# Performance work log

Hardware: AMD Instinct MI355X
Metric: run time of the kernel (lower is better)

## Reference

```python
import jax, jax.numpy as jnp
import numpy as np

D_MODEL = 1024
NUM_HEAD = 16
D_HEAD = D_MODEL // NUM_HEAD
NEG_INF = -1e9


def setup_inputs() -> dict:
    key = jax.random.key(0)
    ks = jax.random.split(key, 10)
    B, S = 16, 512
    v = jax.random.normal(ks[0], (B, S, D_MODEL), dtype=jnp.float32)
    lengths = jax.random.randint(ks[1], (B,), 1, S + 1, dtype=jnp.int32)
    scale = 0.02
    Wq = jax.random.normal(ks[2], (D_MODEL, D_MODEL), dtype=jnp.float32) * scale
    bq = jnp.zeros((D_MODEL,), dtype=jnp.float32)
    Wk = jax.random.normal(ks[3], (D_MODEL, D_MODEL), dtype=jnp.float32) * scale
    bk = jnp.zeros((D_MODEL,), dtype=jnp.float32)
    Wv = jax.random.normal(ks[4], (D_MODEL, D_MODEL), dtype=jnp.float32) * scale
    bv = jnp.zeros((D_MODEL,), dtype=jnp.float32)
    Wo = jax.random.normal(ks[5], (D_MODEL, D_MODEL), dtype=jnp.float32) * scale
    bo = jnp.zeros((D_MODEL,), dtype=jnp.float32)
    return {"v": v, "lengths": lengths, "Wq": Wq, "bq": bq, "Wk": Wk,
            "bk": bk, "Wv": Wv, "bv": bv, "Wo": Wo, "bo": bo}


def reference(v, lengths, Wq, bq, Wk, bk, Wv, bv, Wo, bo):
    B, S, D = v.shape
    H, Dh = NUM_HEAD, D_HEAD
    # key-padding mask: True where key position j is valid (j < lengths[b])
    valid = jnp.arange(S)[None, :] < lengths[:, None]          # [B, S]
    # project q, k, v and split heads -> [B, H, S, Dh]
    def split_heads(x):
        return x.reshape(B, S, H, Dh).transpose(0, 2, 1, 3)
    q = split_heads(v @ Wq + bq)
    k = split_heads(v @ Wk + bk)
    val = split_heads(v @ Wv + bv)
    scores = jnp.einsum('bhqd,bhkd->bhqk', q, k) / jnp.sqrt(jnp.float32(Dh))
    scores = jnp.where(valid[:, None, None, :], scores, NEG_INF)  # mask padded keys
    attn = jax.nn.softmax(scores, axis=-1)
    out = jnp.einsum('bhqk,bhkd->bhqd', attn, val)              # [B, H, S, Dh]
    out = out.transpose(0, 2, 1, 3).reshape(B, S, D)
    return out @ Wo + bo
```

## Files before the change

### kernel.cpp

```cpp
#include <hip/hip_runtime.h>
#include <hip/hip_bf16.h>

typedef unsigned short u16;
typedef __attribute__((ext_vector_type(8))) short short8;
typedef __attribute__((ext_vector_type(4))) float f32x4;

#define B_SZ 16
#define S_SZ 512
#define D_SZ 1024
#define H_SZ 16
#define DH_SZ 64
#define M_SZ (B_SZ * S_SZ)
#define EXPSCALE 0.18033688f

__device__ __forceinline__ void gload_lds16(const void* g, void* l) {
  __builtin_amdgcn_global_load_lds(
      (const __attribute__((address_space(1))) unsigned int*)g,
      (__attribute__((address_space(3))) unsigned int*)l,
      16, 0, 0);
}

__global__ __launch_bounds__(256) void prep(
    const float* __restrict__ v, u16* __restrict__ vB,
    const float* __restrict__ W0, const float* __restrict__ W1,
    const float* __restrict__ W2, const float* __restrict__ W3,
    u16* __restrict__ T0, u16* __restrict__ T1,
    u16* __restrict__ T2, u16* __restrict__ T3) {
  __shared__ float tile[32][33];
  const int bid = blockIdx.x;
  if (bid < 8192) {
    int i = bid * 256 + threadIdx.x;
    const float4 f = *(const float4*)&v[(size_t)i * 4];
    ushort4 o; __hip_bfloat16 h;
    h = __float2bfloat16(f.x); o.x = *(u16*)&h;
    h = __float2bfloat16(f.y); o.y = *(u16*)&h;
    h = __float2bfloat16(f.z); o.z = *(u16*)&h;
    h = __float2bfloat16(f.w); o.w = *(u16*)&h;
    *(ushort4*)&vB[(size_t)i * 4] = o;
    return;
  }
  const int tb = bid - 8192;
  const int z = tb >> 10, rem = tb & 1023;
  const int by = rem >> 5, bx = rem & 31;
  const float* W; u16* T;
  switch (z) {
    case 0: W = W0; T = T0; break;
    case 1: W = W1; T = T1; break;
    case 2: W = W2; T = T2; break;
    default: W = W3; T = T3; break;
  }
  int tx = threadIdx.x & 31, ty = threadIdx.x >> 5;
  int x = bx * 32 + tx;
#pragma unroll
  for (int i = 0; i < 32; i += 8)
    tile[ty + i][tx] = W[(size_t)(by * 32 + ty + i) * 1024 + x];
  __syncthreads();
  int x2 = by * 32 + tx;
#pragma unroll
  for (int i = 0; i < 32; i += 8) {
    __hip_bfloat16 h = __float2bfloat16(tile[tx][ty + i]);
    T[(size_t)(bx * 32 + ty + i) * 1024 + x2] = *(u16*)&h;
  }
}

struct G8 {
  const u16* A; const u16* Bt;
  u16* As; u16* Bs;
  int m0, n0;
  int wave, c, quad, r7, wm, wn;
  int srow, slc8;
};

#define AS_T (128 * 64)
#define BS_T (256 * 64)

__device__ __forceinline__ void stage_a(const G8& g, int buf, int kt, int i) {
  const int grp = g.wave * 2 + i;
  gload_lds16(&g.A[(size_t)(g.m0 + grp * 8 + g.srow) * 1024 + kt * 64 + g.slc8],
              g.As + buf * AS_T + grp * 512);
}
__device__ __forceinline__ void stage_b(const G8& g, int buf, int kt, int i) {
  const int grp = g.wave * 4 + i;
  gload_lds16(&g.Bt[(size_t)(g.n0 + grp * 8 + g.srow) * 1024 + kt * 64 + g.slc8],
              g.Bs + buf * BS_T + grp * 512);
}

template<bool ST, int VM>
__device__ __forceinline__ void tile_step(const G8& g, int cur, int stg, int kt2,
                                          f32x4 acc[4][4]) {
  const u16* ab = g.As + cur * AS_T;
  const u16* bb = g.Bs + cur * BS_T;
  short8 af[4], bf[4];

  {
    const int pc = (g.quad ^ g.r7) * 8;
#pragma unroll
    for (int i = 0; i < 4; ++i) {
      af[i] = *(const short8*)&ab[(g.wm + i * 16 + g.c) * 64 + pc];
      bf[i] = *(const short8*)&bb[(g.wn + i * 16 + g.c) * 64 + pc];
    }
    if constexpr (ST) {
      stage_a(g, stg, kt2, 0);
      stage_a(g, stg, kt2, 1);
      stage_b(g, stg, kt2, 0);
    }
    __builtin_amdgcn_s_barrier();
    __builtin_amdgcn_s_setprio(1);
#pragma unroll
    for (int mi = 0; mi < 4; ++mi)
#pragma unroll
      for (int ni = 0; ni < 4; ++ni)
        acc[mi][ni] = __builtin_amdgcn_mfma_f32_16x16x32_bf16(
            af[mi], bf[ni], acc[mi][ni], 0, 0, 0);
    __builtin_amdgcn_s_setprio(0);
    __builtin_amdgcn_s_barrier();
  }

  {
    const int pc = ((4 + g.quad) ^ g.r7) * 8;
#pragma unroll
    for (int i = 0; i < 4; ++i) {
      af[i] = *(const short8*)&ab[(g.wm + i * 16 + g.c) * 64 + pc];
      bf[i] = *(const short8*)&bb[(g.wn + i * 16 + g.c) * 64 + pc];
    }
    if constexpr (ST) {
      stage_b(g, stg, kt2, 1);
      stage_b(g, stg, kt2, 2);
      stage_b(g, stg, kt2, 3);
    }
    __builtin_amdgcn_s_barrier();
    __builtin_amdgcn_s_setprio(1);
#pragma unroll
    for (int mi = 0; mi < 4; ++mi)
#pragma unroll
      for (int ni = 0; ni < 4; ++ni)
        acc[mi][ni] = __builtin_amdgcn_mfma_f32_16x16x32_bf16(
            af[mi], bf[ni], acc[mi][ni], 0, 0, 0);
    __builtin_amdgcn_s_setprio(0);
    if constexpr (VM == 6) {
      asm volatile("s_waitcnt vmcnt(6)" ::: "memory");
      __builtin_amdgcn_s_barrier();
    } else if constexpr (VM == 0) {
      asm volatile("s_waitcnt vmcnt(0)" ::: "memory");
      __builtin_amdgcn_s_barrier();
    }
  }
}

__device__ __forceinline__ void gemm_core8(
    const u16* __restrict__ A, const u16* __restrict__ Bt,
    u16* AsB, u16* BsB, int m0, int n0, f32x4 acc[4][4]) {
  const int tid = threadIdx.x;
  const int lane = tid & 63;
  G8 g;
  g.A = A; g.Bt = Bt; g.As = AsB; g.Bs = BsB;
  g.m0 = m0; g.n0 = n0;
  g.wave = tid >> 6;
  g.c = lane & 15; g.quad = lane >> 4; g.r7 = g.c & 7;
  g.wm = (g.wave >> 2) * 64;
  g.wn = (g.wave & 3) * 64;
  g.srow = lane >> 3;
  g.slc8 = ((lane & 7) ^ g.srow) * 8;

  stage_a(g, 0, 0, 0); stage_a(g, 0, 0, 1);
  stage_b(g, 0, 0, 0); stage_b(g, 0, 0, 1); stage_b(g, 0, 0, 2); stage_b(g, 0, 0, 3);
  stage_a(g, 1, 1, 0); stage_a(g, 1, 1, 1);
  stage_b(g, 1, 1, 0); stage_b(g, 1, 1, 1); stage_b(g, 1, 1, 2); stage_b(g, 1, 1, 3);
  asm volatile("s_waitcnt vmcnt(6)" ::: "memory");
  __builtin_amdgcn_s_barrier();

  int cur = 0, stg = 2;
#pragma unroll 1
  for (int t = 0; t < 14; ++t) {
    tile_step<true, 6>(g, cur, stg, t + 2, acc);
    cur = (cur == 2) ? 0 : cur + 1;
    stg = (stg == 2) ? 0 : stg + 1;
  }
  tile_step<false, 0>(g, cur, 0, 0, acc);
  tile_step<false, -1>(g, 0, 0, 0, acc);
}

__global__ __launch_bounds__(512, 2) void gemm_qkv(
    const u16* __restrict__ A,
    const u16* __restrict__ BtQ, const u16* __restrict__ BtK, const u16* __restrict__ BtV,
    const float* __restrict__ bq, const float* __restrict__ bk, const float* __restrict__ bv,
    u16* __restrict__ Qo, u16* __restrict__ Kt, u16* __restrict__ Vt) {
  __shared__ u16 As[3][AS_T];
  __shared__ u16 Bs[3][BS_T];
  const int z = blockIdx.z;
  const u16* Bt = (z == 0) ? BtQ : (z == 1) ? BtK : BtV;
  const float* bias = (z == 0) ? bq : (z == 1) ? bk : bv;
  const int m0 = blockIdx.x * 128, n0 = blockIdx.y * 256;

  f32x4 acc[4][4];
#pragma unroll
  for (int i = 0; i < 4; ++i)
#pragma unroll
    for (int j = 0; j < 4; ++j) acc[i][j] = f32x4{0.f, 0.f, 0.f, 0.f};

  gemm_core8(A, Bt, &As[0][0], &Bs[0][0], m0, n0, acc);

  const int lane = threadIdx.x & 63, wave = threadIdx.x >> 6;
  const int wm = (wave >> 2) * 64, wn = (wave & 3) * 64;
  const int c = lane & 15, quad = lane >> 4;
#pragma unroll
  for (int ni = 0; ni < 4; ++ni) {
    int n = n0 + wn + ni * 16 + c;
    float bval = bias[n];
#pragma unroll
    for (int mi = 0; mi < 4; ++mi) {
      int mb = m0 + wm + mi * 16 + quad * 4;
      if (z == 2) {
        int bb = mb >> 9, s = mb & 511, hh = n >> 6, d = n & 63;
        ushort4 st;
        __hip_bfloat16 h0 = __float2bfloat16(acc[mi][ni][0] + bval); st.x = *(u16*)&h0;
        __hip_bfloat16 h1 = __float2bfloat16(acc[mi][ni][1] + bval); st.y = *(u16*)&h1;
        __hip_bfloat16 h2 = __float2bfloat16(acc[mi][ni][2] + bval); st.z = *(u16*)&h2;
        __hip_bfloat16 h3 = __float2bfloat16(acc[mi][ni][3] + bval); st.w = *(u16*)&h3;
        *(ushort4*)&Vt[(((size_t)(bb * 16 + hh) * 64 + d) << 9) + s] = st;
      } else {
#pragma unroll
        for (int r = 0; r < 4; ++r) {
          int m = mb + r;
          float val = acc[mi][ni][r] + bval;
          __hip_bfloat16 hb = __float2bfloat16(val);
          if (z == 0) {
            Qo[(size_t)m * 1024 + n] = *(u16*)&hb;
          } else {
            int bb = m >> 9, s = m & 511, hh = n >> 6, d = n & 63;
            Kt[(((size_t)(bb * 16 + hh) * 512 + s) << 6) + d] = *(u16*)&hb;
          }
        }
      }
    }
  }
}

__global__ __launch_bounds__(512, 2) void gemm_out(
    const u16* __restrict__ A, const u16* __restrict__ Bt,
    const float* __restrict__ bias, float* __restrict__ Cf) {
  __shared__ u16 As[3][AS_T];
  __shared__ u16 Bs[3][BS_T];
  const int m0 = blockIdx.x * 128, n0 = blockIdx.y * 256;

  f32x4 acc[4][4];
#pragma unroll
  for (int i = 0; i < 4; ++i)
#pragma unroll
    for (int j = 0; j < 4; ++j) acc[i][j] = f32x4{0.f, 0.f, 0.f, 0.f};

  gemm_core8(A, Bt, &As[0][0], &Bs[0][0], m0, n0, acc);

  const int lane = threadIdx.x & 63, wave = threadIdx.x >> 6;
  const int wm = (wave >> 2) * 64, wn = (wave & 3) * 64;
  const int c = lane & 15, quad = lane >> 4;
#pragma unroll
  for (int ni = 0; ni < 4; ++ni) {
    int n = n0 + wn + ni * 16 + c;
    float bval = bias[n];
#pragma unroll
    for (int mi = 0; mi < 4; ++mi) {
#pragma unroll
      for (int r = 0; r < 4; ++r) {
        int m = m0 + wm + mi * 16 + quad * 4 + r;
        Cf[(size_t)m * 1024 + n] = acc[mi][ni][r] + bval;
      }
    }
  }
}

__global__ __launch_bounds__(256) void attn_v6(
    const u16* __restrict__ Q, const u16* __restrict__ Kt,
    const u16* __restrict__ Vt, const int* __restrict__ lengths,
    u16* __restrict__ O) {
  const int qc = blockIdx.x, h = blockIdx.y, b = blockIdx.z;
  const int t = threadIdx.x;
  const int lane = t & 63, wave = t >> 6;
  const int c = lane & 15, quad = lane >> 4;
  const int kb = quad * 8;
  const int len = lengths[b];
  const int q0 = qc * 128 + wave * 32;

  __shared__ __align__(16) u16 Ks[64 * 64];
  __shared__ __align__(16) u16 Vs[64 * 64];
  __shared__ __align__(16) u16 Pt[4][32 * 72];

  const size_t bBase = (size_t)b * (S_SZ * D_SZ);
  const size_t hBase = ((size_t)(b * H_SZ + h)) * (S_SZ * DH_SZ);

  short8 aq[2][2];
#pragma unroll
  for (int qt = 0; qt < 2; ++qt) {
    aq[qt][0] = *(const short8*)&Q[bBase + (size_t)(q0 + qt * 16 + c) * 1024 + h * 64 + kb];
    aq[qt][1] = *(const short8*)&Q[bBase + (size_t)(q0 + qt * 16 + c) * 1024 + h * 64 + 32 + kb];
  }

  const int srow = lane >> 3;
  const int slc = (lane & 7) ^ srow;

  float rs[2] = {0.f, 0.f};
  f32x4 o[2][4];
#pragma unroll
  for (int qt = 0; qt < 2; ++qt)
#pragma unroll
    for (int i = 0; i < 4; ++i) o[qt][i] = f32x4{0.f, 0.f, 0.f, 0.f};

  const int kmax = (len + 63) & ~63;
  for (int k0 = 0; k0 < kmax; k0 += 64) {
    __syncthreads();
#pragma unroll
    for (int g = 0; g < 2; ++g) {
      const int rb = (wave * 2 + g) * 8;
      gload_lds16(&Kt[hBase + (size_t)(k0 + rb + srow) * 64 + slc * 8],
                  &Ks[(wave * 2 + g) * 512]);
      gload_lds16(&Vt[hBase + (size_t)(rb + srow) * 512 + k0 + slc * 8],
                  &Vs[(wave * 2 + g) * 512]);
    }
    __syncthreads();

#pragma unroll
    for (int sub = 0; sub < 4; ++sub) {
      const int row = sub * 16 + c;
      short8 bk0 = *(const short8*)&Ks[row * 64 + ((quad ^ (c & 7))) * 8];
      short8 bk1 = *(const short8*)&Ks[row * 64 + (((4 + quad) ^ (c & 7))) * 8];
      const int keyb = k0 + sub * 16 + quad * 4;
#pragma unroll
      for (int qt = 0; qt < 2; ++qt) {
        f32x4 s = {0.f, 0.f, 0.f, 0.f};
        s = __builtin_amdgcn_mfma_f32_16x16x32_bf16(bk0, aq[qt][0], s, 0, 0, 0);
        s = __builtin_amdgcn_mfma_f32_16x16x32_bf16(bk1, aq[qt][1], s, 0, 0, 0);
        ushort4 st;
        float p0 = (keyb + 0) < len ? exp2f(s[0] * EXPSCALE) : 0.f;
        float p1 = (keyb + 1) < len ? exp2f(s[1] * EXPSCALE) : 0.f;
        float p2 = (keyb + 2) < len ? exp2f(s[2] * EXPSCALE) : 0.f;
        float p3 = (keyb + 3) < len ? exp2f(s[3] * EXPSCALE) : 0.f;
        __hip_bfloat16 h0 = __float2bfloat16(p0); st.x = *(u16*)&h0;
        __hip_bfloat16 h1 = __float2bfloat16(p1); st.y = *(u16*)&h1;
        __hip_bfloat16 h2 = __float2bfloat16(p2); st.z = *(u16*)&h2;
        __hip_bfloat16 h3 = __float2bfloat16(p3); st.w = *(u16*)&h3;
        rs[qt] += __bfloat162float(h0) + __bfloat162float(h1) +
                  __bfloat162float(h2) + __bfloat162float(h3);
        *(ushort4*)&Pt[wave][(qt * 16 + c) * 72 + sub * 16 + quad * 4] = st;
      }
    }
#pragma unroll
    for (int ksub = 0; ksub < 2; ++ksub) {
      const short8 pa0 = *(const short8*)&Pt[wave][(c) * 72 + ksub * 32 + kb];
      const short8 pa1 = *(const short8*)&Pt[wave][(16 + c) * 72 + ksub * 32 + kb];
#pragma unroll
      for (int dt = 0; dt < 4; ++dt) {
        const int vrow = dt * 16 + c;
        short8 vb = *(const short8*)&Vs[vrow * 64 + (((ksub * 4 + quad) ^ (c & 7))) * 8];
        o[0][dt] = __builtin_amdgcn_mfma_f32_16x16x32_bf16(pa0, vb, o[0][dt], 0, 0, 0);
        o[1][dt] = __builtin_amdgcn_mfma_f32_16x16x32_bf16(pa1, vb, o[1][dt], 0, 0, 0);
      }
    }
  }

#pragma unroll
  for (int qt = 0; qt < 2; ++qt) {
    rs[qt] += __shfl_xor(rs[qt], 16, 64);
    rs[qt] += __shfl_xor(rs[qt], 32, 64);
  }

#pragma unroll
  for (int qt = 0; qt < 2; ++qt) {
    float lq[4];
#pragma unroll
    for (int r = 0; r < 4; ++r) lq[r] = __shfl(rs[qt], quad * 4 + r, 16);
#pragma unroll
    for (int dt = 0; dt < 4; ++dt) {
#pragma unroll
      for (int r = 0; r < 4; ++r) {
        int s = q0 + qt * 16 + quad * 4 + r;
        float val = o[qt][dt][r] / lq[r];
        __hip_bfloat16 ob = __float2bfloat16(val);
        O[bBase + (size_t)s * 1024 + h * 64 + dt * 16 + c] = *(u16*)&ob;
      }
    }
  }
}

extern "C" void kernel_launch(void* const* d_in, const int* in_sizes, int n_in,
                              void* d_out, int out_size, void* d_ws, size_t ws_size,
                              hipStream_t stream) {
  const float* v  = (const float*)d_in[0];
  const int* lengths = (const int*)d_in[1];
  const float* Wq = (const float*)d_in[2];
  const float* bq = (const float*)d_in[3];
  const float* Wk = (const float*)d_in[4];
  const float* bk = (const float*)d_in[5];
  const float* Wv = (const float*)d_in[6];
  const float* bv = (const float*)d_in[7];
  const float* Wo = (const float*)d_in[8];
  const float* bo = (const float*)d_in[9];

  char* ws = (char*)d_ws;
  const size_t TSZ = (size_t)M_SZ * D_SZ * 2;
  const size_t WSZ = (size_t)1 << 21;
  u16* vB  = (u16*)(ws);
  u16* AO  = vB;
  u16* WqT = (u16*)(ws + TSZ + 0 * WSZ);
  u16* WkT = (u16*)(ws + TSZ + 1 * WSZ);
  u16* WvT = (u16*)(ws + TSZ + 2 * WSZ);
  u16* WoT = (u16*)(ws + TSZ + 3 * WSZ);
  u16* Qb  = (u16*)(ws + TSZ + 4 * WSZ + 0 * TSZ);
  u16* Kt  = (u16*)(ws + TSZ + 4 * WSZ + 1 * TSZ);
  u16* Vt  = (u16*)(ws + TSZ + 4 * WSZ + 2 * TSZ);

  prep<<<dim3(8192 + 4096), 256, 0, stream>>>(v, vB, Wq, Wk, Wv, Wo, WqT, WkT, WvT, WoT);

  gemm_qkv<<<dim3(64, 4, 3), 512, 0, stream>>>(vB, WqT, WkT, WvT, bq, bk, bv, Qb, Kt, Vt);

  attn_v6<<<dim3(4, 16, 16), 256, 0, stream>>>(Qb, Kt, Vt, lengths, AO);

  gemm_out<<<dim3(64, 4), 512, 0, stream>>>(AO, WoT, bo, (float*)d_out);
}
```

Measured before the change: 220.5 us.

## Double-buffer K/V tiles in attention kernel with prefetch and manual waitcnt

The attention kernel now keeps two LDS buffers for K and V and issues the global-to-LDS loads for the next key tile before computing on the current one. It replaces the two __syncthreads per iteration with a partial vmcnt wait plus raw s_barrier, and raises wave priority around the PV MFMA block. The aim is to hide global load latency behind the QK and PV math. In exchange it doubles K/V LDS use, which may reduce occupancy, and the hand-written vmcnt counts must match the number of loads in flight.

```diff
diff --git a/kernel.cpp b/kernel.cpp
--- a/kernel.cpp
+++ b/kernel.cpp
@@ -18,6 +18,10 @@
       (const __attribute__((address_space(1))) unsigned int*)g,
       (__attribute__((address_space(3))) unsigned int*)l,
       16, 0, 0);
+}
+
+__device__ __forceinline__ void fenced_barrier() {
+  asm volatile("s_barrier" ::: "memory");
 }
 
 __global__ __launch_bounds__(256) void prep(
@@ -269,7 +273,20 @@
   }
 }
 
-__global__ __launch_bounds__(256) void attn_v6(
+__device__ __forceinline__ void attn_stage(
+    const u16* __restrict__ Kt, const u16* __restrict__ Vt, size_t hBase,
+    int wave, int srow, int slc, int k0, u16* KsB, u16* VsB) {
+#pragma unroll
+  for (int g = 0; g < 2; ++g) {
+    const int rb = (wave * 2 + g) * 8;
+    gload_lds16(&Kt[hBase + (size_t)(k0 + rb + srow) * 64 + slc * 8],
+                &KsB[(wave * 2 + g) * 512]);
+    gload_lds16(&Vt[hBase + (size_t)(rb + srow) * 512 + k0 + slc * 8],
+                &VsB[(wave * 2 + g) * 512]);
+  }
+}
+
+__global__ __launch_bounds__(256) void attn_v7(
     const u16* __restrict__ Q, const u16* __restrict__ Kt,
     const u16* __restrict__ Vt, const int* __restrict__ lengths,
     u16* __restrict__ O) {
@@ -281,8 +298,8 @@
   const int len = lengths[b];
   const int q0 = qc * 128 + wave * 32;
 
-  __shared__ __align__(16) u16 Ks[64 * 64];
-  __shared__ __align__(16) u16 Vs[64 * 64];
+  __shared__ __align__(16) u16 Ks[2][64 * 64];
+  __shared__ __align__(16) u16 Vs[2][64 * 64];
   __shared__ __align__(16) u16 Pt[4][32 * 72];
 
   const size_t bBase = (size_t)b * (S_SZ * D_SZ);
@@ -306,23 +323,29 @@
     for (int i = 0; i < 4; ++i) o[qt][i] = f32x4{0.f, 0.f, 0.f, 0.f};
 
   const int kmax = (len + 63) & ~63;
-  for (int k0 = 0; k0 < kmax; k0 += 64) {
-    __syncthreads();
-#pragma unroll
-    for (int g = 0; g < 2; ++g) {
-      const int rb = (wave * 2 + g) * 8;
-      gload_lds16(&Kt[hBase + (size_t)(k0 + rb + srow) * 64 + slc * 8],
-                  &Ks[(wave * 2 + g) * 512]);
-      gload_lds16(&Vt[hBase + (size_t)(rb + srow) * 512 + k0 + slc * 8],
-                  &Vs[(wave * 2 + g) * 512]);
-    }
-    __syncthreads();
+  const int nt = kmax >> 6;
+
+  attn_stage(Kt, Vt, hBase, wave, srow, slc, 0, &Ks[0][0], &Vs[0][0]);
+
+#pragma unroll 1
+  for (int tt = 0; tt < nt; ++tt) {
+    const int k0 = tt << 6;
+    if (tt + 1 < nt) {
+      attn_stage(Kt, Vt, hBase, wave, srow, slc, k0 + 64,
+                 &Ks[(tt + 1) & 1][0], &Vs[(tt + 1) & 1][0]);
+      asm volatile("s_waitcnt vmcnt(4)" ::: "memory");
+    } else {
+      asm volatile("s_waitcnt vmcnt(0)" ::: "memory");
+    }
+    fenced_barrier();
+    const u16* KsC = &Ks[tt & 1][0];
+    const u16* VsC = &Vs[tt & 1][0];
 
 #pragma unroll
     for (int sub = 0; sub < 4; ++sub) {
       const int row = sub * 16 + c;
-      short8 bk0 = *(const short8*)&Ks[row * 64 + ((quad ^ (c & 7))) * 8];
-      short8 bk1 = *(const short8*)&Ks[row * 64 + (((4 + quad) ^ (c & 7))) * 8];
+      short8 bk0 = *(const short8*)&KsC[row * 64 + ((quad ^ (c & 7))) * 8];
+      short8 bk1 = *(const short8*)&KsC[row * 64 + (((4 + quad) ^ (c & 7))) * 8];
       const int keyb = k0 + sub * 16 + quad * 4;
 #pragma unroll
       for (int qt = 0; qt < 2; ++qt) {
@@ -343,6 +366,7 @@
         *(ushort4*)&Pt[wave][(qt * 16 + c) * 72 + sub * 16 + quad * 4] = st;
       }
     }
+    __builtin_amdgcn_s_setprio(1);
 #pragma unroll
     for (int ksub = 0; ksub < 2; ++ksub) {
       const short8 pa0 = *(const short8*)&Pt[wave][(c) * 72 + ksub * 32 + kb];
@@ -350,11 +374,13 @@
 #pragma unroll
       for (int dt = 0; dt < 4; ++dt) {
         const int vrow = dt * 16 + c;
-        short8 vb = *(const short8*)&Vs[vrow * 64 + (((ksub * 4 + quad) ^ (c & 7))) * 8];
+        short8 vb = *(const short8*)&VsC[vrow * 64 + (((ksub * 4 + quad) ^ (c & 7))) * 8];
         o[0][dt] = __builtin_amdgcn_mfma_f32_16x16x32_bf16(pa0, vb, o[0][dt], 0, 0, 0);
         o[1][dt] = __builtin_amdgcn_mfma_f32_16x16x32_bf16(pa1, vb, o[1][dt], 0, 0, 0);
       }
     }
+    __builtin_amdgcn_s_setprio(0);
+    fenced_barrier();
   }
 
 #pragma unroll
@@ -412,7 +438,7 @@
 
   gemm_qkv<<<dim3(64, 4, 3), 512, 0, stream>>>(vB, WqT, WkT, WvT, bq, bk, bv, Qb, Kt, Vt);
 
-  attn_v6<<<dim3(4, 16, 16), 256, 0, stream>>>(Qb, Kt, Vt, lengths, AO);
+  attn_v7<<<dim3(4, 16, 16), 256, 0, stream>>>(Qb, Kt, Vt, lengths, AO);
 
   gemm_out<<<dim3(64, 4), 512, 0, stream>>>(AO, WoT, bo, (float*)d_out);
 }
```

New measurement: 225.1 us. +2.1%, slower.
